# Kernel optimization log

Hardware: AMD Instinct MI355X
Metric: run time of the kernel (lower is better)

Reference implementation:

```python
import jax, jax.numpy as jnp
import numpy as np
import math

B, L, D = 4, 4096, 1024
PI = math.pi
LN_EPS = 1e-5


def setup_inputs() -> dict:
    key = jax.random.key(0)
    ks = jax.random.split(key, 16)
    s = 1.0 / math.sqrt(D)
    inp = {
        "x": jax.random.normal(ks[0], (B, L, D), dtype=jnp.float32),
        # Linear weights stored as [in, out] (torch W.T)
        "Wk": jax.random.normal(ks[1], (D, D), dtype=jnp.float32) * s,
        "bk": jnp.zeros((D,), dtype=jnp.float32),
        "Wq": jax.random.normal(ks[2], (D, D), dtype=jnp.float32) * s,
        "bq": jnp.zeros((D,), dtype=jnp.float32),
        "Wv": jax.random.normal(ks[3], (D, D), dtype=jnp.float32) * s,
        "bv": jnp.zeros((D,), dtype=jnp.float32),
        "ln_g": jnp.ones((D,), dtype=jnp.float32),
        "ln_b": jnp.zeros((D,), dtype=jnp.float32),
        "Wo": jax.random.normal(ks[4], (D, D), dtype=jnp.float32) * s,
        "bo": jnp.zeros((D,), dtype=jnp.float32),
        "Wg1": jax.random.normal(ks[5], (D, D // 4), dtype=jnp.float32) * s,
        "bg1": jnp.zeros((D // 4,), dtype=jnp.float32),
        "Wg2": jax.random.normal(ks[6], (D // 4, 1), dtype=jnp.float32) * (2.0 / math.sqrt(D)),
        "bg2": jnp.zeros((1,), dtype=jnp.float32),
        "pos_phases": jax.random.normal(ks[7], (L, D), dtype=jnp.float32) * PI,
    }
    return inp


def _layernorm(x, g, b):
    mu = jnp.mean(x, axis=-1, keepdims=True)
    var = jnp.var(x, axis=-1, keepdims=True)
    return (x - mu) * jax.lax.rsqrt(var + LN_EPS) * g + b


def reference(x, Wk, bk, Wq, bq, Wv, bv, ln_g, ln_b, Wo, bo, Wg1, bg1, Wg2, bg2, pos_phases):
    # dropout is identity in eval mode
    key_phases = jnp.tanh(x @ Wk + bk) * PI          # [B,L,D]
    query_phases = jnp.tanh(x @ Wq + bq) * PI        # [B,L,D]
    V = x @ Wv + bv                                   # [B,L,D]

    cos_k, sin_k = jnp.cos(key_phases), jnp.sin(key_phases)
    cos_q, sin_q = jnp.cos(query_phases), jnp.sin(query_phases)

    mem_real = jnp.cumsum(V * cos_k, axis=1)
    mem_imag = jnp.cumsum(V * sin_k, axis=1)
    content_retrieved = mem_real * cos_q + mem_imag * sin_q

    pp = pos_phases[: x.shape[1]]                     # [L,D]
    cos_p, sin_p = jnp.cos(pp), jnp.sin(pp)
    pos_mem_real = jnp.cumsum(V * cos_p, axis=1)
    pos_mem_imag = jnp.cumsum(V * sin_p, axis=1)
    pos_retrieved = pos_mem_real * cos_p + pos_mem_imag * sin_p

    gate = jax.nn.sigmoid(jax.nn.gelu(x @ Wg1 + bg1) @ Wg2 + bg2)  # [B,L,1]
    combined = gate * content_retrieved + (1.0 - gate) * pos_retrieved

    positions = jnp.arange(1, x.shape[1] + 1, dtype=jnp.float32)
    norm = jnp.sqrt(positions)[None, :, None]
    out = _layernorm(combined / norm, ln_g, ln_b) @ Wo + bo
    return x + out
```

## Files before the change

### kernel.cpp

```cpp
#include <hip/hip_runtime.h>
#include <math.h>

#define B_ 4
#define L_ 4096
#define D_ 1024
#define DG_ 256
#define NC_ 128
#define CL_ 32
#define PI_F 3.14159265358979323846f
#define LN_EPS_F 1e-5f

typedef __attribute__((ext_vector_type(8))) _Float16 f16x8;
typedef __attribute__((ext_vector_type(8))) short s16x8;
typedef __attribute__((ext_vector_type(4))) short s16x4;
typedef __attribute__((ext_vector_type(4))) float f32x4;

__device__ inline short f2h(float f) { return __builtin_bit_cast(short, (_Float16)f); }
__device__ inline float h2f(short s) { return (float)__builtin_bit_cast(_Float16, s); }

__device__ inline float ftanh(float x) {
    float e = __expf(2.0f * x);
    return 1.0f - 2.0f / (e + 1.0f);
}
__device__ inline void fsincos(float x, float* s, float* c) {
    *s = __sinf(x); *c = __cosf(x);
}

__device__ inline void gld16(const void* g, void* l) {
    __builtin_amdgcn_global_load_lds(
        (const __attribute__((address_space(1))) unsigned int*)g,
        (__attribute__((address_space(3))) unsigned int*)l, 16, 0, 0);
}

__global__ __launch_bounds__(256)
void conv_x(const float* __restrict__ x, short* __restrict__ xh, int n8)
{
    int t = blockIdx.x * 256 + threadIdx.x;
    if (t >= n8) return;
    const float4* p = (const float4*)x + (size_t)t * 2;
    float4 a = p[0], b = p[1];
    s16x8 v;
    v[0] = f2h(a.x); v[1] = f2h(a.y); v[2] = f2h(a.z); v[3] = f2h(a.w);
    v[4] = f2h(b.x); v[5] = f2h(b.y); v[6] = f2h(b.z); v[7] = f2h(b.w);
    *(s16x8*)(xh + (size_t)t * 8) = v;
}

__global__ __launch_bounds__(256)
void convT(const float* __restrict__ W, short* __restrict__ Th, int N)
{
    __shared__ float tile[64][65];
    const int n0 = blockIdx.x * 64, k0 = blockIdx.y * 64;
    const int t = threadIdx.x;
    const int r = t >> 4, c4 = (t & 15) * 4;

    #pragma unroll
    for (int i = 0; i < 4; ++i) {
        float4 v = *(const float4*)&W[(size_t)(k0 + r + i * 16) * N + n0 + c4];
        tile[r + i * 16][c4 + 0] = v.x;
        tile[r + i * 16][c4 + 1] = v.y;
        tile[r + i * 16][c4 + 2] = v.z;
        tile[r + i * 16][c4 + 3] = v.w;
    }
    __syncthreads();
    #pragma unroll
    for (int i = 0; i < 4; ++i) {
        const int n = r + i * 16;
        s16x4 o;
        o[0] = f2h(tile[c4 + 0][n]);
        o[1] = f2h(tile[c4 + 1][n]);
        o[2] = f2h(tile[c4 + 2][n]);
        o[3] = f2h(tile[c4 + 3][n]);
        *(s16x4*)&Th[(size_t)(n0 + n) * 1024 + k0 + c4] = o;
    }
}

#define SBAR() __builtin_amdgcn_sched_barrier(0)
#define BARRIER() do { SBAR(); __builtin_amdgcn_s_barrier(); SBAR(); } while (0)
#define PRIO1() __builtin_amdgcn_s_setprio(1)
#define PRIO0() __builtin_amdgcn_s_setprio(0)
#define LGKM0() do { asm volatile("s_waitcnt lgkmcnt(0)" ::: "memory"); \
                     __builtin_amdgcn_sched_barrier(0); } while (0)

#define DSR(dst, areg, OFS)                                              \
    asm volatile("ds_read_b128 %0, %1 offset:" OFS                       \
                 : "=v"(dst) : "v"(areg))

#define RDA4(areg)                                                       \
    DSR(af[0], areg, "0");    DSR(af[1], areg, "2048");                  \
    DSR(af[2], areg, "4096"); DSR(af[3], areg, "6144");
#define RDA4H(areg)                                                      \
    DSR(af[0], areg, "8192");  DSR(af[1], areg, "10240");                \
    DSR(af[2], areg, "12288"); DSR(af[3], areg, "14336");
#define RDB4(areg, KK)                                                   \
    DSR(bq[0][KK], areg, "0");    DSR(bq[1][KK], areg, "2048");          \
    DSR(bq[2][KK], areg, "4096"); DSR(bq[3][KK], areg, "6144");

#define MF(MG, KK)                                                       \
    _Pragma("unroll") for (int i_ = 0; i_ < 4; ++i_)                     \
    _Pragma("unroll") for (int n_ = 0; n_ < 4; ++n_)                     \
        acc[(MG)*4 + i_][n_] = __builtin_amdgcn_mfma_f32_16x16x32_f16(   \
            af[i_], bq[n_][KK], acc[(MG)*4 + i_][n_], 0, 0, 0);

template<int EPI, typename OT>
__global__ __launch_bounds__(512, 2)
void mgemm256(const short* __restrict__ A, const short* __restrict__ Bt,
              const float* __restrict__ X, OT* __restrict__ out0,
              short* __restrict__ out1, short* __restrict__ out2,
              const float* __restrict__ b0, const float* __restrict__ b1,
              const float* __restrict__ b2, int M, int N, int K)
{
    extern __shared__ char lds[];

    const int tid = threadIdx.x;
    const int w = tid >> 6, l = tid & 63;
    const int wr = w >> 2, wc = w & 3;
    const int fr = l & 15, kb = l >> 4;
    const int bm = blockIdx.x * 256, bn = blockIdx.y * 256;
    const int np = K >> 7;

    const int s = fr & 7;
    const int cK0 = (((s >> 2) & 1) << 6) | (((kb ^ s) & 3) << 4);
    const int aA0 = (wr << 14) + fr * 128 + cK0;
    const int aA1 = aA0 ^ 64;
    const int aB0 = 32768 + ((wc >> 1) << 14) + ((wc & 1) * 64 + fr) * 128 + cK0;
    const int aB1 = aB0 ^ 64;
    const int aA0o = aA0 + 65536, aA1o = aA1 + 65536;
    const int aB0o = aB0 + 65536, aB1o = aB1 + 65536;

    const int p0 = tid * 16;
    const int sr = p0 >> 7;
    const int sc = (p0 & 127) ^ ((sr & 7) << 4);
    const short* gA = A  + (size_t)(bm + sr) * K + (sc >> 1);
    const short* gB = Bt + (size_t)(bn + sr) * K + (sc >> 1);
    char* ldst = lds + (w << 10);
    const size_t q1 = (size_t)64 * K, q2 = 2 * q1, q3 = 3 * q1;

    f32x4 acc[8][4] = {};
    f16x8 af[4];
    f16x8 bq[4][2];

    gld16(gA,      ldst);          gld16(gA + q1, ldst + 8192);
    gld16(gA + q2, ldst + 16384);  gld16(gA + q3, ldst + 24576);
    gld16(gB,      ldst + 32768);  gld16(gB + q1, ldst + 40960);
    gld16(gB + q2, ldst + 49152);  gld16(gB + q3, ldst + 57344);
    gld16(gA +      64, ldst + 65536);
    gld16(gA + q2 + 64, ldst + 65536 + 16384);
    asm volatile("s_waitcnt vmcnt(2)" ::: "memory");
    BARRIER();

    const short* gAn = gA + 64;
    const short* gBn = gB + 64;

    for (int pp = 0; pp < np; ++pp) {
        const bool nl = (pp + 1 < np);

        RDA4(aA0); RDB4(aB0, 0);
        gld16(gBn,      ldst + 98304);         gld16(gBn + q1, ldst + 98304 + 8192);
        gld16(gBn + q2, ldst + 98304 + 16384); gld16(gBn + q3, ldst + 98304 + 24576);
        BARRIER();
        LGKM0();
        PRIO1(); MF(0, 0); PRIO0();
        BARRIER();
        RDA4(aA1); RDB4(aB1, 1);
        gld16(gAn + q1, ldst + 65536 + 8192);
        gld16(gAn + q3, ldst + 65536 + 24576);
        BARRIER();
        LGKM0();
        PRIO1(); MF(0, 1); PRIO0();
        BARRIER();
        RDA4H(aA0);
        BARRIER();
        LGKM0();
        PRIO1(); MF(1, 0); PRIO0();
        BARRIER();
        RDA4H(aA1);
        if (nl) { gld16(gAn + 64, ldst); gld16(gAn + 64 + q2, ldst + 16384); }
        BARRIER();
        LGKM0();
        PRIO1(); MF(1, 1); PRIO0();
        SBAR();
        asm volatile("s_waitcnt vmcnt(2)" ::: "memory");
        __builtin_amdgcn_s_barrier(); SBAR();

        RDA4(aA0o); RDB4(aB0o, 0);
        if (nl) {
            gld16(gBn +      64, ldst + 32768); gld16(gBn + q1 + 64, ldst + 40960);
            gld16(gBn + q2 + 64, ldst + 49152); gld16(gBn + q3 + 64, ldst + 57344);
        }
        BARRIER();
        LGKM0();
        PRIO1(); MF(0, 0); PRIO0();
        BARRIER();
        RDA4(aA1o); RDB4(aB1o, 1);
        if (nl) {
            gld16(gAn + q1 + 64, ldst + 8192);
            gld16(gAn + q3 + 64, ldst + 24576);
        }
        BARRIER();
        LGKM0();
        PRIO1(); MF(0, 1); PRIO0();
        BARRIER();
        if (!nl) asm volatile("s_waitcnt vmcnt(0)" ::: "memory");
        RDA4H(aA0o);
        BARRIER();
        LGKM0();
        PRIO1(); MF(1, 0); PRIO0();
        BARRIER();
        RDA4H(aA1o);
        if (nl) { gld16(gAn + 128, ldst + 65536); gld16(gAn + 128 + q2, ldst + 65536 + 16384); }
        BARRIER();
        LGKM0();
        PRIO1(); MF(1, 1); PRIO0();
        SBAR();
        if (nl) {
            asm volatile("s_waitcnt vmcnt(2)" ::: "memory");
            __builtin_amdgcn_s_barrier(); SBAR();
        }
        gAn += 128; gBn += 128;
    }

    if constexpr (EPI == 4) {
        short* op; const float* bp; bool dt;
        if (bn < 1024)      { op = (short*)out0; bp = b0; dt = true;  }
        else if (bn < 2048) { op = out1;         bp = b1; dt = true;  }
        else                { op = out2;         bp = b2; dt = false; }
        const int cb = bn & 1023;
        float bc[4];
        #pragma unroll
        for (int nf = 0; nf < 4; ++nf) bc[nf] = bp[cb + wc * 64 + nf * 16 + fr];
        #pragma unroll
        for (int mf = 0; mf < 8; ++mf)
            #pragma unroll
            for (int rr = 0; rr < 4; ++rr) {
                const int row = bm + wr * 128 + mf * 16 + kb * 4 + rr;
                #pragma unroll
                for (int nf = 0; nf < 4; ++nf) {
                    const int cc = cb + wc * 64 + nf * 16 + fr;
                    float c = acc[mf][nf][rr] + bc[nf];
                    if (dt) c = ftanh(c) * PI_F;
                    op[(size_t)row * 1024 + cc] = f2h(c);
                }
            }
    } else {
        float bc[4];
        #pragma unroll
        for (int nf = 0; nf < 4; ++nf) bc[nf] = b0[bn + wc * 64 + nf * 16 + fr];
        #pragma unroll
        for (int mf = 0; mf < 8; ++mf)
            #pragma unroll
            for (int rr = 0; rr < 4; ++rr) {
                const int row = bm + wr * 128 + mf * 16 + kb * 4 + rr;
                #pragma unroll
                for (int nf = 0; nf < 4; ++nf) {
                    const int col = bn + wc * 64 + nf * 16 + fr;
                    float c = acc[mf][nf][rr] + bc[nf] + X[(size_t)row * N + col];
                    ((float*)out0)[(size_t)row * N + col] = c;
                }
            }
    }
}

template<int EPI>
__global__ __launch_bounds__(256)
void mgemm(const short* __restrict__ A, const short* __restrict__ Bt,
           short* __restrict__ out0, const float* __restrict__ b0,
           int M, int N, int K)
{
    __shared__ __align__(16) short As[128 * 32];
    __shared__ __align__(16) short Bs[128 * 32];

    const int tid = threadIdx.x;
    const int w  = tid >> 6, l = tid & 63;
    const int wr = w >> 1,  wc = w & 1;
    const int fr = l & 15,  kb = l >> 4;
    const int bm = blockIdx.x * 128, bn = blockIdx.y * 128;

    const int srow = l >> 2;
    const int scol = (l & 3) * 8;
    const short* gA0 = A  + (size_t)(bm + w * 32 +  0 + srow) * K + scol;
    const short* gA1 = A  + (size_t)(bm + w * 32 + 16 + srow) * K + scol;
    const short* gB0 = Bt + (size_t)(bn + w * 32 +  0 + srow) * K + scol;
    const short* gB1 = Bt + (size_t)(bn + w * 32 + 16 + srow) * K + scol;
    short* lA0 = &As[(w * 32 +  0) * 32];
    short* lA1 = &As[(w * 32 + 16) * 32];
    short* lB0 = &Bs[(w * 32 +  0) * 32];
    short* lB1 = &Bs[(w * 32 + 16) * 32];

    f32x4 acc[4][4] = {};

    for (int k0 = 0; k0 < K; k0 += 32) {
        gld16(gA0 + k0, lA0); gld16(gA1 + k0, lA1);
        gld16(gB0 + k0, lB0); gld16(gB1 + k0, lB1);
        __syncthreads();

        f16x8 afr[4], bfr[4];
        #pragma unroll
        for (int m = 0; m < 4; ++m)
            afr[m] = *(const f16x8*)&As[(wr * 64 + m * 16 + fr) * 32 + kb * 8];
        #pragma unroll
        for (int n = 0; n < 4; ++n)
            bfr[n] = *(const f16x8*)&Bs[(wc * 64 + n * 16 + fr) * 32 + kb * 8];
        #pragma unroll
        for (int m = 0; m < 4; ++m)
            #pragma unroll
            for (int n = 0; n < 4; ++n)
                acc[m][n] = __builtin_amdgcn_mfma_f32_16x16x32_f16(afr[m], bfr[n], acc[m][n], 0, 0, 0);
        __syncthreads();
    }

    #pragma unroll
    for (int n = 0; n < 4; ++n) {
        const int col = bn + wc * 64 + n * 16 + fr;
        const float bcol = b0[col];
        #pragma unroll
        for (int m = 0; m < 4; ++m)
            #pragma unroll
            for (int r = 0; r < 4; ++r) {
                const int row = bm + wr * 64 + m * 16 + kb * 4 + r;
                float c = acc[m][n][r] + bcol;
                float tt = 0.7978845608028654f * (c + 0.044715f * c * c * c);
                c = 0.5f * c * (1.0f + ftanh(tt));
                out0[(size_t)row * N + col] = f2h(c);
            }
    }
}

__global__ __launch_bounds__(256)
void gate_kernel(const short* __restrict__ H, const float* __restrict__ Wg2,
                 const float* __restrict__ bg2, float* __restrict__ gate)
{
    const int wid = threadIdx.x >> 6;
    const int lane = threadIdx.x & 63;
    const int row = blockIdx.x * 4 + wid;
    s16x4 hv = *(const s16x4*)&H[(size_t)row * DG_ + lane * 4];
    float4 wv = *(const float4*)&Wg2[lane * 4];
    float s = h2f(hv[0]) * wv.x + h2f(hv[1]) * wv.y + h2f(hv[2]) * wv.z + h2f(hv[3]) * wv.w;
    #pragma unroll
    for (int o = 32; o; o >>= 1) s += __shfl_down(s, o);
    if (lane == 0) gate[row] = 1.0f / (1.0f + __expf(-(s + bg2[0])));
}

__global__ __launch_bounds__(256)
void passA(const short* __restrict__ V, const short* __restrict__ KP,
           const float* __restrict__ PP, f32x4* __restrict__ SI)
{
    const int bid = blockIdx.x;
    const int b = bid >> 7, c = bid & 127;
    const int d0 = threadIdx.x * 4;

    f32x4 cr = {}, ci = {}, pr = {}, pi = {};
    const size_t base  = ((size_t)b * L_ + (size_t)c * CL_) * D_ + d0;
    const size_t pbase = (size_t)c * CL_ * D_ + d0;
    for (int ll = 0; ll < CL_; ++ll) {
        s16x4 v4  = *(const s16x4*)&V [base + (size_t)ll * D_];
        s16x4 kp4 = *(const s16x4*)&KP[base + (size_t)ll * D_];
        f32x4 pp4 = *(const f32x4*)&PP[pbase + (size_t)ll * D_];
        #pragma unroll
        for (int j = 0; j < 4; ++j) {
            float v = h2f(v4[j]);
            float sk, ck, sp, cp;
            fsincos(h2f(kp4[j]), &sk, &ck);
            fsincos(pp4[j], &sp, &cp);
            cr[j] += v * ck; ci[j] += v * sk;
            pr[j] += v * cp; pi[j] += v * sp;
        }
    }
    const size_t sidx = ((size_t)bid << 10) + d0;
    #pragma unroll
    for (int j = 0; j < 4; ++j) {
        f32x4 o = { cr[j], ci[j], pr[j], pi[j] };
        SI[sidx + j] = o;
    }
}

__global__ __launch_bounds__(256)
void passB(f32x4* __restrict__ SI)
{
    const int t = blockIdx.x * 256 + threadIdx.x;
    const int b = t >> 10, d = t & 1023;
    f32x4 run = {};
    for (int c = 0; c < NC_; ++c) {
        const size_t idx = ((size_t)(b * NC_ + c) << 10) + d;
        f32x4 v = SI[idx];
        SI[idx] = run;
        run += v;
    }
}

__global__ __launch_bounds__(256)
void passC(const short* __restrict__ V, const short* KP,
           const short* __restrict__ QP, const float* __restrict__ PP,
           const float* __restrict__ gate, const f32x4* __restrict__ SI,
           const float* __restrict__ ln_g, const float* __restrict__ ln_b,
           short* Yb)
{
    const int bid = blockIdx.x;
    const int b = bid >> 7, c = bid & 127;
    const int d0 = threadIdx.x * 4;

    const size_t sidx = ((size_t)bid << 10) + d0;
    f32x4 cr, ci, pr, pi;
    #pragma unroll
    for (int j = 0; j < 4; ++j) {
        f32x4 s = SI[sidx + j];
        cr[j] = s[0]; ci[j] = s[1]; pr[j] = s[2]; pi[j] = s[3];
    }
    const f32x4 g_ln = *(const f32x4*)&ln_g[d0];
    const f32x4 b_ln = *(const f32x4*)&ln_b[d0];

    __shared__ float2 lred[2][4];
    const int wid = threadIdx.x >> 6;
    const int lane = threadIdx.x & 63;

    for (int l0 = 0; l0 < CL_; ++l0) {
        const int ll = c * CL_ + l0;
        const size_t off = ((size_t)b * L_ + ll) * D_ + d0;
        s16x4 v4  = *(const s16x4*)&V [off];
        s16x4 kp4 = *(const s16x4*)&KP[off];
        s16x4 qp4 = *(const s16x4*)&QP[off];
        f32x4 pp4 = *(const f32x4*)&PP[(size_t)ll * D_ + d0];
        const float gv = gate[b * L_ + ll];
        const float rs_pos = rsqrtf((float)(ll + 1));

        f32x4 u;
        #pragma unroll
        for (int j = 0; j < 4; ++j) {
            float v = h2f(v4[j]);
            float sk, ck, sq, cq, sp, cp;
            fsincos(h2f(kp4[j]), &sk, &ck);
            fsincos(h2f(qp4[j]), &sq, &cq);
            fsincos(pp4[j], &sp, &cp);
            cr[j] += v * ck; ci[j] += v * sk;
            pr[j] += v * cp; pi[j] += v * sp;
            float content = cr[j] * cq + ci[j] * sq;
            float posr    = pr[j] * cp + pi[j] * sp;
            u[j] = (gv * content + (1.0f - gv) * posr) * rs_pos;
        }

        float s  = u[0] + u[1] + u[2] + u[3];
        float s2 = u[0]*u[0] + u[1]*u[1] + u[2]*u[2] + u[3]*u[3];
        #pragma unroll
        for (int o = 32; o; o >>= 1) {
            s  += __shfl_down(s, o);
            s2 += __shfl_down(s2, o);
        }
        const int pb = l0 & 1;
        if (lane == 0) lred[pb][wid] = make_float2(s, s2);
        __syncthreads();
        float ts  = lred[pb][0].x + lred[pb][1].x + lred[pb][2].x + lred[pb][3].x;
        float ts2 = lred[pb][0].y + lred[pb][1].y + lred[pb][2].y + lred[pb][3].y;
        const float mu  = ts * (1.0f / D_);
        const float var = ts2 * (1.0f / D_) - mu * mu;
        const float rsv = rsqrtf(var + LN_EPS_F);
        s16x4 yo;
        #pragma unroll
        for (int j = 0; j < 4; ++j)
            yo[j] = f2h((u[j] - mu) * rsv * g_ln[j] + b_ln[j]);
        *(s16x4*)&Yb[off] = yo;
    }
}

extern "C" void kernel_launch(void* const* d_in, const int* in_sizes, int n_in,
                              void* d_out, int out_size, void* d_ws, size_t ws_size,
                              hipStream_t stream)
{
    const float* x    = (const float*)d_in[0];
    const float* Wk   = (const float*)d_in[1];
    const float* bk   = (const float*)d_in[2];
    const float* Wq   = (const float*)d_in[3];
    const float* bq   = (const float*)d_in[4];
    const float* Wv   = (const float*)d_in[5];
    const float* bv   = (const float*)d_in[6];
    const float* ln_g = (const float*)d_in[7];
    const float* ln_b = (const float*)d_in[8];
    const float* Wo   = (const float*)d_in[9];
    const float* bo   = (const float*)d_in[10];
    const float* Wg1  = (const float*)d_in[11];
    const float* bg1  = (const float*)d_in[12];
    const float* Wg2  = (const float*)d_in[13];
    const float* bg2  = (const float*)d_in[14];
    const float* PP   = (const float*)d_in[15];

    float* out = (float*)d_out;

    const size_t BLD   = (size_t)B_ * L_ * D_;
    const size_t SZ_X  = BLD * 2;
    const size_t SZ_R1 = (size_t)B_ * L_ * DG_ * 2;
    const size_t SZ_G1 = (size_t)D_ * DG_ * 2;
    const size_t NEED  = SZ_X + SZ_R1 + SZ_G1 + 3 * SZ_X;
    if (ws_size < NEED) {
        hipMemcpyAsync(d_out, d_in[0], BLD * sizeof(float),
                       hipMemcpyDeviceToDevice, stream);
        return;
    }

    char* wsb = (char*)d_ws;
    short* xh   = (short*)(wsb);
    char*  r1   = wsb + SZ_X;
    short* Wcat = (short*)r1;
    short* H    = (short*)r1;
    short* Wg1T = (short*)(r1 + SZ_R1);
    short* KP   = (short*)(r1 + SZ_R1 + SZ_G1);
    short* QP   = (short*)((char*)KP + SZ_X);
    short* V    = (short*)((char*)QP + SZ_X);
    float* gate = (float*)(wsb);
    short* WtO  = (short*)(wsb + 65536);
    f32x4* SI   = (f32x4*)(wsb + 65536 + 2097152);
    short* Yb   = KP;

    const int M = B_ * L_;
    dim3 blk(256);

    conv_x<<<(int)(BLD / 8 / 256), blk, 0, stream>>>(x, xh, (int)(BLD / 8));
    dim3 gT(D_ / 64, 16);
    dim3 gTg(DG_ / 64, 16);
    convT<<<gT, blk, 0, stream>>>(Wk, Wcat + 0 * D_ * D_, D_);
    convT<<<gT, blk, 0, stream>>>(Wq, Wcat + 1 * D_ * D_, D_);
    convT<<<gT, blk, 0, stream>>>(Wv, Wcat + 2 * D_ * D_, D_);
    convT<<<gTg, blk, 0, stream>>>(Wg1, Wg1T, DG_);

    dim3 gQKV(M / 256, 3072 / 256);
    dim3 gH(M / 128, DG_ / 128);
    hipLaunchKernelGGL((mgemm256<4, short>), gQKV, dim3(512), 131072, stream,
                       xh, Wcat, nullptr, KP, QP, V, bk, bq, bv, M, 3072, D_);
    hipLaunchKernelGGL((mgemm<2>), gH, blk, 0, stream,
                       xh, Wg1T, H, bg1, M, DG_, D_);

    gate_kernel<<<M / 4, blk, 0, stream>>>(H, Wg2, bg2, gate);
    convT<<<gT, blk, 0, stream>>>(Wo, WtO, D_);

    passA<<<B_ * NC_, blk, 0, stream>>>(V, KP, PP, SI);
    passB<<<(B_ * D_) / 256, blk, 0, stream>>>(SI);
    passC<<<B_ * NC_, blk, 0, stream>>>(V, KP, QP, PP, gate, SI, ln_g, ln_b, Yb);

    dim3 gO(M / 256, D_ / 256);
    hipLaunchKernelGGL((mgemm256<3, float>), gO, dim3(512), 131072, stream,
                       Yb, WtO, x, out, nullptr, nullptr, bo, nullptr, nullptr,
                       M, D_, D_);
}
```

Baseline: 301.6 us.

## Fuse gate GEMM and GELU-dot reduction into the QKV GEMM launch

Appends the transposed Wg1 as an extra 256-column block to the concatenated QKV weight, so the large 256x256 GEMM also computes the gate hidden layer. Its epilogue applies GELU, multiplies by Wg2, reduces across lanes and atomically accumulates a per-row pre-sigmoid gate; passC then adds bg2 and applies the sigmoid. This removes the separate small GEMM, the H intermediate round trip and the gate kernel launch, at the cost of a memset, float atomics and a non-uniform extra column of tiles. The B-tile global loads in the main loop are also split across two MFMA phases to spread memory issue.

```diff
diff --git a/kernel.cpp b/kernel.cpp
--- a/kernel.cpp
+++ b/kernel.cpp
@@ -107,7 +107,9 @@
               const float* __restrict__ X, OT* __restrict__ out0,
               short* __restrict__ out1, short* __restrict__ out2,
               const float* __restrict__ b0, const float* __restrict__ b1,
-              const float* __restrict__ b2, int M, int N, int K)
+              const float* __restrict__ b2, const float* __restrict__ bg1p,
+              const float* __restrict__ wg2p, float* __restrict__ gatep,
+              int M, int N, int K)
 {
     extern __shared__ char lds[];
 
@@ -155,20 +157,22 @@
         const bool nl = (pp + 1 < np);
 
         RDA4(aA0); RDB4(aB0, 0);
-        gld16(gBn,      ldst + 98304);         gld16(gBn + q1, ldst + 98304 + 8192);
-        gld16(gBn + q2, ldst + 98304 + 16384); gld16(gBn + q3, ldst + 98304 + 24576);
+        gld16(gBn,      ldst + 98304);
+        gld16(gBn + q1, ldst + 98304 + 8192);
         BARRIER();
         LGKM0();
         PRIO1(); MF(0, 0); PRIO0();
         BARRIER();
         RDA4(aA1); RDB4(aB1, 1);
+        gld16(gBn + q2, ldst + 98304 + 16384);
+        gld16(gBn + q3, ldst + 98304 + 24576);
+        BARRIER();
+        LGKM0();
+        PRIO1(); MF(0, 1); PRIO0();
+        BARRIER();
+        RDA4H(aA0);
         gld16(gAn + q1, ldst + 65536 + 8192);
         gld16(gAn + q3, ldst + 65536 + 24576);
-        BARRIER();
-        LGKM0();
-        PRIO1(); MF(0, 1); PRIO0();
-        BARRIER();
-        RDA4H(aA0);
         BARRIER();
         LGKM0();
         PRIO1(); MF(1, 0); PRIO0();
@@ -184,24 +188,28 @@
 
         RDA4(aA0o); RDB4(aB0o, 0);
         if (nl) {
-            gld16(gBn +      64, ldst + 32768); gld16(gBn + q1 + 64, ldst + 40960);
-            gld16(gBn + q2 + 64, ldst + 49152); gld16(gBn + q3 + 64, ldst + 57344);
+            gld16(gBn +      64, ldst + 32768);
+            gld16(gBn + q1 + 64, ldst + 40960);
         }
         BARRIER();
         LGKM0();
         PRIO1(); MF(0, 0); PRIO0();
         BARRIER();
         RDA4(aA1o); RDB4(aB1o, 1);
+        if (nl) {
+            gld16(gBn + q2 + 64, ldst + 49152);
+            gld16(gBn + q3 + 64, ldst + 57344);
+        }
+        BARRIER();
+        LGKM0();
+        PRIO1(); MF(0, 1); PRIO0();
+        BARRIER();
+        if (!nl) asm volatile("s_waitcnt vmcnt(0)" ::: "memory");
+        RDA4H(aA0o);
         if (nl) {
             gld16(gAn + q1 + 64, ldst + 8192);
             gld16(gAn + q3 + 64, ldst + 24576);
         }
-        BARRIER();
-        LGKM0();
-        PRIO1(); MF(0, 1); PRIO0();
-        BARRIER();
-        if (!nl) asm volatile("s_waitcnt vmcnt(0)" ::: "memory");
-        RDA4H(aA0o);
         BARRIER();
         LGKM0();
         PRIO1(); MF(1, 0); PRIO0();
@@ -220,27 +228,56 @@
     }
 
     if constexpr (EPI == 4) {
-        short* op; const float* bp; bool dt;
-        if (bn < 1024)      { op = (short*)out0; bp = b0; dt = true;  }
-        else if (bn < 2048) { op = out1;         bp = b1; dt = true;  }
-        else                { op = out2;         bp = b2; dt = false; }
-        const int cb = bn & 1023;
-        float bc[4];
-        #pragma unroll
-        for (int nf = 0; nf < 4; ++nf) bc[nf] = bp[cb + wc * 64 + nf * 16 + fr];
-        #pragma unroll
-        for (int mf = 0; mf < 8; ++mf)
+        if (bn < 3072) {
+            short* op; const float* bp; bool dt;
+            if (bn < 1024)      { op = (short*)out0; bp = b0; dt = true;  }
+            else if (bn < 2048) { op = out1;         bp = b1; dt = true;  }
+            else                { op = out2;         bp = b2; dt = false; }
+            const int cb = bn & 1023;
+            float bc[4];
             #pragma unroll
-            for (int rr = 0; rr < 4; ++rr) {
-                const int row = bm + wr * 128 + mf * 16 + kb * 4 + rr;
+            for (int nf = 0; nf < 4; ++nf) bc[nf] = bp[cb + wc * 64 + nf * 16 + fr];
+            #pragma unroll
+            for (int mf = 0; mf < 8; ++mf)
                 #pragma unroll
-                for (int nf = 0; nf < 4; ++nf) {
-                    const int cc = cb + wc * 64 + nf * 16 + fr;
-                    float c = acc[mf][nf][rr] + bc[nf];
-                    if (dt) c = ftanh(c) * PI_F;
-                    op[(size_t)row * 1024 + cc] = f2h(c);
+                for (int rr = 0; rr < 4; ++rr) {
+                    const int row = bm + wr * 128 + mf * 16 + kb * 4 + rr;
+                    #pragma unroll
+                    for (int nf = 0; nf < 4; ++nf) {
+                        const int cc = cb + wc * 64 + nf * 16 + fr;
+                        float c = acc[mf][nf][rr] + bc[nf];
+                        if (dt) c = ftanh(c) * PI_F;
+                        op[(size_t)row * 1024 + cc] = f2h(c);
+                    }
                 }
+        } else {
+            float bg[4], wg[4];
+            #pragma unroll
+            for (int nf = 0; nf < 4; ++nf) {
+                const int cl = wc * 64 + nf * 16 + fr;
+                bg[nf] = bg1p[cl];
+                wg[nf] = wg2p[cl];
             }
+            #pragma unroll
+            for (int mf = 0; mf < 8; ++mf)
+                #pragma unroll
+                for (int rr = 0; rr < 4; ++rr) {
+                    const int row = bm + wr * 128 + mf * 16 + kb * 4 + rr;
+                    float part = 0.f;
+                    #pragma unroll
+                    for (int nf = 0; nf < 4; ++nf) {
+                        float c = acc[mf][nf][rr] + bg[nf];
+                        float tt = 0.7978845608028654f * (c + 0.044715f * c * c * c);
+                        float g = 0.5f * c * (1.0f + ftanh(tt));
+                        part += g * wg[nf];
+                    }
+                    part += __shfl_xor(part, 1);
+                    part += __shfl_xor(part, 2);
+                    part += __shfl_xor(part, 4);
+                    part += __shfl_xor(part, 8);
+                    if (fr == 0) atomicAdd(&gatep[row], part);
+                }
+        }
     } else {
         float bc[4];
         #pragma unroll
@@ -260,86 +297,6 @@
     }
 }
 
-template<int EPI>
-__global__ __launch_bounds__(256)
-void mgemm(const short* __restrict__ A, const short* __restrict__ Bt,
-           short* __restrict__ out0, const float* __restrict__ b0,
-           int M, int N, int K)
-{
-    __shared__ __align__(16) short As[128 * 32];
-    __shared__ __align__(16) short Bs[128 * 32];
-
-    const int tid = threadIdx.x;
-    const int w  = tid >> 6, l = tid & 63;
-    const int wr = w >> 1,  wc = w & 1;
-    const int fr = l & 15,  kb = l >> 4;
-    const int bm = blockIdx.x * 128, bn = blockIdx.y * 128;
-
-    const int srow = l >> 2;
-    const int scol = (l & 3) * 8;
-    const short* gA0 = A  + (size_t)(bm + w * 32 +  0 + srow) * K + scol;
-    const short* gA1 = A  + (size_t)(bm + w * 32 + 16 + srow) * K + scol;
-    const short* gB0 = Bt + (size_t)(bn + w * 32 +  0 + srow) * K + scol;
-    const short* gB1 = Bt + (size_t)(bn + w * 32 + 16 + srow) * K + scol;
-    short* lA0 = &As[(w * 32 +  0) * 32];
-    short* lA1 = &As[(w * 32 + 16) * 32];
-    short* lB0 = &Bs[(w * 32 +  0) * 32];
-    short* lB1 = &Bs[(w * 32 + 16) * 32];
-
-    f32x4 acc[4][4] = {};
-
-    for (int k0 = 0; k0 < K; k0 += 32) {
-        gld16(gA0 + k0, lA0); gld16(gA1 + k0, lA1);
-        gld16(gB0 + k0, lB0); gld16(gB1 + k0, lB1);
-        __syncthreads();
-
-        f16x8 afr[4], bfr[4];
-        #pragma unroll
-        for (int m = 0; m < 4; ++m)
-            afr[m] = *(const f16x8*)&As[(wr * 64 + m * 16 + fr) * 32 + kb * 8];
-        #pragma unroll
-        for (int n = 0; n < 4; ++n)
-            bfr[n] = *(const f16x8*)&Bs[(wc * 64 + n * 16 + fr) * 32 + kb * 8];
-        #pragma unroll
-        for (int m = 0; m < 4; ++m)
-            #pragma unroll
-            for (int n = 0; n < 4; ++n)
-                acc[m][n] = __builtin_amdgcn_mfma_f32_16x16x32_f16(afr[m], bfr[n], acc[m][n], 0, 0, 0);
-        __syncthreads();
-    }
-
-    #pragma unroll
-    for (int n = 0; n < 4; ++n) {
-        const int col = bn + wc * 64 + n * 16 + fr;
-        const float bcol = b0[col];
-        #pragma unroll
-        for (int m = 0; m < 4; ++m)
-            #pragma unroll
-            for (int r = 0; r < 4; ++r) {
-                const int row = bm + wr * 64 + m * 16 + kb * 4 + r;
-                float c = acc[m][n][r] + bcol;
-                float tt = 0.7978845608028654f * (c + 0.044715f * c * c * c);
-                c = 0.5f * c * (1.0f + ftanh(tt));
-                out0[(size_t)row * N + col] = f2h(c);
-            }
-    }
-}
-
-__global__ __launch_bounds__(256)
-void gate_kernel(const short* __restrict__ H, const float* __restrict__ Wg2,
-                 const float* __restrict__ bg2, float* __restrict__ gate)
-{
-    const int wid = threadIdx.x >> 6;
-    const int lane = threadIdx.x & 63;
-    const int row = blockIdx.x * 4 + wid;
-    s16x4 hv = *(const s16x4*)&H[(size_t)row * DG_ + lane * 4];
-    float4 wv = *(const float4*)&Wg2[lane * 4];
-    float s = h2f(hv[0]) * wv.x + h2f(hv[1]) * wv.y + h2f(hv[2]) * wv.z + h2f(hv[3]) * wv.w;
-    #pragma unroll
-    for (int o = 32; o; o >>= 1) s += __shfl_down(s, o);
-    if (lane == 0) gate[row] = 1.0f / (1.0f + __expf(-(s + bg2[0])));
-}
-
 __global__ __launch_bounds__(256)
 void passA(const short* __restrict__ V, const short* __restrict__ KP,
            const float* __restrict__ PP, f32x4* __restrict__ SI)
@@ -390,9 +347,9 @@
 __global__ __launch_bounds__(256)
 void passC(const short* __restrict__ V, const short* KP,
            const short* __restrict__ QP, const float* __restrict__ PP,
-           const float* __restrict__ gate, const f32x4* __restrict__ SI,
-           const float* __restrict__ ln_g, const float* __restrict__ ln_b,
-           short* Yb)
+           const float* __restrict__ gatep, const float* __restrict__ bg2,
+           const f32x4* __restrict__ SI, const float* __restrict__ ln_g,
+           const float* __restrict__ ln_b, short* Yb)
 {
     const int bid = blockIdx.x;
     const int b = bid >> 7, c = bid & 127;
@@ -407,6 +364,7 @@
     }
     const f32x4 g_ln = *(const f32x4*)&ln_g[d0];
     const f32x4 b_ln = *(const f32x4*)&ln_b[d0];
+    const float bg2v = bg2[0];
 
     __shared__ float2 lred[2][4];
     const int wid = threadIdx.x >> 6;
@@ -419,7 +377,7 @@
         s16x4 kp4 = *(const s16x4*)&KP[off];
         s16x4 qp4 = *(const s16x4*)&QP[off];
         f32x4 pp4 = *(const f32x4*)&PP[(size_t)ll * D_ + d0];
-        const float gv = gate[b * L_ + ll];
+        const float gv = 1.0f / (1.0f + __expf(-(gatep[b * L_ + ll] + bg2v)));
         const float rs_pos = rsqrtf((float)(ll + 1));
 
         f32x4 u;
@@ -486,8 +444,8 @@
     const size_t BLD   = (size_t)B_ * L_ * D_;
     const size_t SZ_X  = BLD * 2;
     const size_t SZ_R1 = (size_t)B_ * L_ * DG_ * 2;
-    const size_t SZ_G1 = (size_t)D_ * DG_ * 2;
-    const size_t NEED  = SZ_X + SZ_R1 + SZ_G1 + 3 * SZ_X;
+    const size_t SZ_GT = (size_t)B_ * L_ * 4;
+    const size_t NEED  = SZ_X + SZ_R1 + 3 * SZ_X + SZ_GT;
     if (ws_size < NEED) {
         hipMemcpyAsync(d_out, d_in[0], BLD * sizeof(float),
                        hipMemcpyDeviceToDevice, stream);
@@ -498,14 +456,12 @@
     short* xh   = (short*)(wsb);
     char*  r1   = wsb + SZ_X;
     short* Wcat = (short*)r1;
-    short* H    = (short*)r1;
-    short* Wg1T = (short*)(r1 + SZ_R1);
-    short* KP   = (short*)(r1 + SZ_R1 + SZ_G1);
+    short* KP   = (short*)(r1 + SZ_R1);
     short* QP   = (short*)((char*)KP + SZ_X);
     short* V    = (short*)((char*)QP + SZ_X);
-    float* gate = (float*)(wsb);
-    short* WtO  = (short*)(wsb + 65536);
-    f32x4* SI   = (f32x4*)(wsb + 65536 + 2097152);
+    float* gatep = (float*)((char*)V + SZ_X);
+    short* WtO  = (short*)(wsb);
+    f32x4* SI   = (f32x4*)(wsb + 2097152);
     short* Yb   = KP;
 
     const int M = B_ * L_;
@@ -514,27 +470,26 @@
     conv_x<<<(int)(BLD / 8 / 256), blk, 0, stream>>>(x, xh, (int)(BLD / 8));
     dim3 gT(D_ / 64, 16);
     dim3 gTg(DG_ / 64, 16);
-    convT<<<gT, blk, 0, stream>>>(Wk, Wcat + 0 * D_ * D_, D_);
-    convT<<<gT, blk, 0, stream>>>(Wq, Wcat + 1 * D_ * D_, D_);
-    convT<<<gT, blk, 0, stream>>>(Wv, Wcat + 2 * D_ * D_, D_);
-    convT<<<gTg, blk, 0, stream>>>(Wg1, Wg1T, DG_);
-
-    dim3 gQKV(M / 256, 3072 / 256);
-    dim3 gH(M / 128, DG_ / 128);
+    convT<<<gT, blk, 0, stream>>>(Wk, Wcat + (size_t)0 * D_ * D_, D_);
+    convT<<<gT, blk, 0, stream>>>(Wq, Wcat + (size_t)1 * D_ * D_, D_);
+    convT<<<gT, blk, 0, stream>>>(Wv, Wcat + (size_t)2 * D_ * D_, D_);
+    convT<<<gTg, blk, 0, stream>>>(Wg1, Wcat + (size_t)3 * D_ * D_, DG_);
+
+    hipMemsetAsync(gatep, 0, SZ_GT, stream);
+    dim3 gQKV(M / 256, 3328 / 256);
     hipLaunchKernelGGL((mgemm256<4, short>), gQKV, dim3(512), 131072, stream,
-                       xh, Wcat, nullptr, KP, QP, V, bk, bq, bv, M, 3072, D_);
-    hipLaunchKernelGGL((mgemm<2>), gH, blk, 0, stream,
-                       xh, Wg1T, H, bg1, M, DG_, D_);
-
-    gate_kernel<<<M / 4, blk, 0, stream>>>(H, Wg2, bg2, gate);
+                       xh, Wcat, nullptr, KP, QP, V, bk, bq, bv,
+                       bg1, Wg2, gatep, M, 3328, D_);
+
     convT<<<gT, blk, 0, stream>>>(Wo, WtO, D_);
 
     passA<<<B_ * NC_, blk, 0, stream>>>(V, KP, PP, SI);
     passB<<<(B_ * D_) / 256, blk, 0, stream>>>(SI);
-    passC<<<B_ * NC_, blk, 0, stream>>>(V, KP, QP, PP, gate, SI, ln_g, ln_b, Yb);
+    passC<<<B_ * NC_, blk, 0, stream>>>(V, KP, QP, PP, gatep, bg2, SI,
+                                        ln_g, ln_b, Yb);
 
     dim3 gO(M / 256, D_ / 256);
     hipLaunchKernelGGL((mgemm256<3, float>), gO, dim3(512), 131072, stream,
                        Yb, WtO, x, out, nullptr, nullptr, bo, nullptr, nullptr,
-                       M, D_, D_);
-}
+                       nullptr, nullptr, nullptr, M, D_, D_);
+}
```

New measurement: 309.2 us. 1.03x slower.
